# Kernel tuning notes

Hardware: AMD Instinct MI355X
Metric: run time of the kernel (lower is better)

The kernel has to match this reference:

```python
import jax, jax.numpy as jnp
import numpy as np

B, N, C, IN, H, G, OUT = 128, 256, 4, 64, 128, 8, 1
NUM_GNN_LAYERS = 2  # num_layers - 1


def setup_inputs() -> dict:
    key = jax.random.key(0)
    k1, k2, k3, k4, k5, k6 = jax.random.split(key, 6)
    V = jax.random.normal(k1, (B, N, IN), dtype=jnp.float32)
    A = jax.random.uniform(k2, (B, N, C, N), dtype=jnp.float32)
    mol_size = jax.random.randint(k3, (B,), 16, N + 1)  # at least 16 real nodes
    W_in = jax.random.normal(k4, (2, H, IN, G), dtype=jnp.float32) / np.float32(np.sqrt(IN) * np.sqrt(G))
    W_g = jax.random.normal(k5, (NUM_GNN_LAYERS, 2, H, H, G), dtype=jnp.float32) / np.float32(np.sqrt(H) * np.sqrt(G))
    W_out = jax.random.normal(k6, (2, OUT, H, 1), dtype=jnp.float32) / np.float32(np.sqrt(H))
    b_out = jnp.zeros((1, OUT), dtype=jnp.float32)
    return {"V": V, "A": A, "mol_size": mol_size, "W_in": W_in, "W_g": W_g, "W_out": W_out, "b_out": b_out}


def _kan_linear(x, W, bias=None):
    # x: [..., in], W: [2, out, in, grid]
    g = W.shape[-1]
    k = jnp.arange(1, g + 1, dtype=x.dtype)  # [g]
    xk = x[..., None] * k                    # [..., in, g]
    y = jnp.einsum('...ik,oik->...o', jnp.cos(xk), W[0]) \
      + jnp.einsum('...ik,oik->...o', jnp.sin(xk), W[1])
    if bias is not None:
        y = y + bias
    return y


def _kan_gnn_layer(h, A, W):
    # h: [b,n,in], A: [b,n,c,m], W: [2,out,in,grid]
    g = W.shape[-1]
    k = jnp.arange(1, g + 1, dtype=h.dtype)
    xk = h[..., None] * k                      # [b,n,in,g]
    f = jnp.einsum('bnik,oik->bno', jnp.cos(xk), W[0]) \
      + jnp.einsum('bnik,oik->bno', jnp.sin(xk), W[1])  # fourier_feat [b,n,out]
    # torch chain permute/reshape/bmm/sum(c) == sum_{n,c} A[b,n,c,m] * f[b,n,o]
    return jnp.einsum('bncm,bno->bmo', A, f)   # [b,m,out]


def reference(V, A, mol_size, W_in, W_g, W_out, b_out):
    h = _kan_linear(V, W_in)                   # [B,N,H]
    for i in range(W_g.shape[0]):
        m = _kan_gnn_layer(h, A, W_g[i])
        h = jax.nn.leaky_relu(m + h, negative_slope=0.01)
    # avg pooling over the first mol_size[i] (real) nodes per graph
    node_mask = (jnp.arange(N) < mol_size[:, None]).astype(h.dtype)  # [B,N]
    summed = jnp.einsum('bnh,bn->bh', h, node_mask)
    y = summed / mol_size[:, None].astype(h.dtype)                    # [B,H]
    out = jax.nn.sigmoid(_kan_linear(y, W_out, b_out))                # [B,OUT]
    return out
```

## Files before the change

kernel.cpp:

```cpp
#include <hip/hip_runtime.h>
#include <math.h>

namespace {
constexpr int B_ = 128;
constexpr int N_ = 256;
constexpr int H_ = 128;
constexpr int M_TOTAL = B_ * N_;
}

#define AS1 __attribute__((address_space(1)))
#define AS3 __attribute__((address_space(3)))

__device__ __forceinline__ void gl_lds16(const float* g, float* l) {
  __builtin_amdgcn_global_load_lds((const AS1 unsigned int*)g,
                                   (AS3 unsigned int*)l, 16, 0, 0);
}

template<int I, int O>
__global__ __launch_bounds__(256)
void wtr_kernel(const float* __restrict__ in, float* __restrict__ out) {
  int idx = blockIdx.x * 256 + threadIdx.x;
  constexpr int TOTAL = 2 * O * I * 8;
  if (idx >= TOTAL) return;
  int g = idx & 7;
  int t = idx >> 3;
  int i = t % I;
  int t2 = t / I;
  int o = t2 % O;
  int s = t2 / O;
  out[(size_t)((i * 8 + g) * 2 + s) * O + o] = in[idx];
}

template<int IN>
__global__ __launch_bounds__(256, 4)
void fourier3(const float* __restrict__ x,
              const float* __restrict__ Wt,
              float* __restrict__ out)
{
  constexpr int PAIRS = IN * 8;
  constexpr int CHUNKS = PAIRS / 16;
  __shared__ alignas(16) float wl[2][16][2][128];
  __shared__ alignas(16) float fC[2][16][64];
  __shared__ alignas(16) float fS[2][16][64];

  const int tid = threadIdx.x;
  const int node0 = blockIdx.x * 64;
  const int og = tid & 15;
  const int ng = tid >> 4;
  const int lane = tid & 63;
  const int wave = tid >> 6;
  const int il = tid >> 6;
  const int nd = tid & 63;

  float acc[4][8];
  #pragma unroll
  for (int a = 0; a < 4; ++a)
    #pragma unroll
    for (int b = 0; b < 8; ++b) acc[a][b] = 0.f;

  float xnext = 0.f;
  if (tid < 128) {
    float xv = x[(size_t)(node0 + nd) * IN + il];
    float s1, c1;
    sincosf(xv, &s1, &c1);
    float ckm = 1.f, skm = 0.f, ck = c1, sk = s1;
    #pragma unroll
    for (int g = 0; g < 8; ++g) {
      fC[0][il * 8 + g][nd] = ck;
      fS[0][il * 8 + g][nd] = sk;
      float cn = 2.f * c1 * ck - ckm, sn = 2.f * c1 * sk - skm;
      ckm = ck; skm = sk; ck = cn; sk = sn;
    }
    if (CHUNKS > 1) xnext = x[(size_t)(node0 + nd) * IN + 2 + il];
  } else {
    const int wv = wave - 2;
    #pragma unroll
    for (int q = 0; q < 8; ++q) {
      int u = (wv * 8 + q) * 64 + lane;
      gl_lds16(Wt + (size_t)u * 4,
               &wl[0][0][0][0] + (size_t)(wv * 8 + q) * 256);
    }
  }
  __syncthreads();

  int p = 0;
  for (int ic = 0; ic < CHUNKS; ++ic) {
    const int pn = p ^ 1;
    const bool more = (ic + 1 < CHUNKS);
    if (more) {
      if (tid < 128) {
        float s1, c1;
        sincosf(xnext, &s1, &c1);
        float ckm = 1.f, skm = 0.f, ck = c1, sk = s1;
        #pragma unroll
        for (int g = 0; g < 8; ++g) {
          fC[pn][il * 8 + g][nd] = ck;
          fS[pn][il * 8 + g][nd] = sk;
          float cn = 2.f * c1 * ck - ckm, sn = 2.f * c1 * sk - skm;
          ckm = ck; skm = sk; ck = cn; sk = sn;
        }
        if (ic + 2 < CHUNKS)
          xnext = x[(size_t)(node0 + nd) * IN + (ic + 2) * 2 + il];
      } else {
        const int wv = wave - 2;
        const float* wsrc = Wt + (size_t)(ic + 1) * 4096;
        float* wdst = &wl[pn][0][0][0];
        #pragma unroll
        for (int q = 0; q < 8; ++q) {
          int u = (wv * 8 + q) * 64 + lane;
          gl_lds16(wsrc + (size_t)u * 4, wdst + (size_t)(wv * 8 + q) * 256);
        }
      }
    }
    #pragma unroll 2
    for (int j = 0; j < 16; ++j) {
      float4 fc = *(const float4*)&fC[p][j][ng * 4];
      float4 fs = *(const float4*)&fS[p][j][ng * 4];
      float4 w0a = *(const float4*)&wl[p][j][0][og * 4];
      float4 w0b = *(const float4*)&wl[p][j][0][og * 4 + 64];
      float4 w1a = *(const float4*)&wl[p][j][1][og * 4];
      float4 w1b = *(const float4*)&wl[p][j][1][og * 4 + 64];
      float fcv[4] = {fc.x, fc.y, fc.z, fc.w};
      float fsv[4] = {fs.x, fs.y, fs.z, fs.w};
      float wa0[4] = {w0a.x, w0a.y, w0a.z, w0a.w};
      float wb0[4] = {w0b.x, w0b.y, w0b.z, w0b.w};
      float wa1[4] = {w1a.x, w1a.y, w1a.z, w1a.w};
      float wb1[4] = {w1b.x, w1b.y, w1b.z, w1b.w};
      #pragma unroll
      for (int nd2 = 0; nd2 < 4; ++nd2) {
        #pragma unroll
        for (int oo = 0; oo < 4; ++oo) {
          acc[nd2][oo]     += fcv[nd2] * wa0[oo] + fsv[nd2] * wa1[oo];
          acc[nd2][4 + oo] += fcv[nd2] * wb0[oo] + fsv[nd2] * wb1[oo];
        }
      }
    }
    __syncthreads();
    p ^= 1;
  }

  #pragma unroll
  for (int nd2 = 0; nd2 < 4; ++nd2) {
    int row = node0 + ng * 4 + nd2;
    float4 ra = {acc[nd2][0], acc[nd2][1], acc[nd2][2], acc[nd2][3]};
    float4 rb = {acc[nd2][4], acc[nd2][5], acc[nd2][6], acc[nd2][7]};
    *(float4*)&out[(size_t)row * H_ + og * 4] = ra;
    *(float4*)&out[(size_t)row * H_ + og * 4 + 64] = rb;
  }
}

__global__ __launch_bounds__(256)
void agg2(const float* __restrict__ A,
          const float* __restrict__ f,
          const float* __restrict__ h_in,
          float* __restrict__ h_out)
{
  __shared__ alignas(16) float As[2][32][64];
  __shared__ alignas(16) float fsh[2][8][128];
  const int tid = threadIdx.x;
  const int b = blockIdx.x >> 2;
  const int m0 = (blockIdx.x & 3) * 64;
  const int og = tid & 15;
  const int mg = tid >> 4;
  const int wave = tid >> 6;

  float acc[4][8];
  #pragma unroll
  for (int i = 0; i < 4; ++i)
    #pragma unroll
    for (int j = 0; j < 8; ++j) acc[i][j] = 0.f;

  const float* Ab = A + (size_t)b * (N_ * 4 * N_) + m0;
  const float* fb = f + (size_t)b * (N_ * H_);

  #pragma unroll
  for (int q = 0; q < 2; ++q) {
    int v = q * 256 + tid;
    gl_lds16(Ab + (size_t)(v >> 4) * N_ + (v & 15) * 4,
             &As[0][0][0] + (size_t)(q * 256 + wave * 64) * 4);
  }
  gl_lds16(fb + (size_t)(tid >> 5) * H_ + (tid & 31) * 4,
           &fsh[0][0][0] + (size_t)(wave * 64) * 4);
  __syncthreads();

  int p = 0;
  for (int ch = 0; ch < 32; ++ch) {
    const int pn = p ^ 1;
    if (ch + 1 < 32) {
      const float* Asrc = Ab + (size_t)(ch + 1) * 32 * N_;
      #pragma unroll
      for (int q = 0; q < 2; ++q) {
        int v = q * 256 + tid;
        gl_lds16(Asrc + (size_t)(v >> 4) * N_ + (v & 15) * 4,
                 &As[pn][0][0] + (size_t)(q * 256 + wave * 64) * 4);
      }
      gl_lds16(fb + (size_t)((ch + 1) * 8 + (tid >> 5)) * H_ + (tid & 31) * 4,
               &fsh[pn][0][0] + (size_t)(wave * 64) * 4);
    }
    #pragma unroll
    for (int kk = 0; kk < 32; ++kk) {
      float4 a  = *(const float4*)&As[p][kk][mg * 4];
      float4 f0 = *(const float4*)&fsh[p][kk >> 2][og * 4];
      float4 f1 = *(const float4*)&fsh[p][kk >> 2][og * 4 + 64];
      float av[4] = {a.x, a.y, a.z, a.w};
      float fo[8] = {f0.x, f0.y, f0.z, f0.w, f1.x, f1.y, f1.z, f1.w};
      #pragma unroll
      for (int mi = 0; mi < 4; ++mi)
        #pragma unroll
        for (int oi = 0; oi < 8; ++oi)
          acc[mi][oi] += av[mi] * fo[oi];
    }
    __syncthreads();
    p ^= 1;
  }

  #pragma unroll
  for (int mi = 0; mi < 4; ++mi) {
    int row = b * N_ + m0 + mg * 4 + mi;
    const float* hr = &h_in[(size_t)row * H_];
    float* ho = &h_out[(size_t)row * H_];
    float4 r0 = *(const float4*)&hr[og * 4];
    float4 r1 = *(const float4*)&hr[og * 4 + 64];
    float4 o0, o1;
    float v;
    v = acc[mi][0] + r0.x; o0.x = v >= 0.f ? v : 0.01f * v;
    v = acc[mi][1] + r0.y; o0.y = v >= 0.f ? v : 0.01f * v;
    v = acc[mi][2] + r0.z; o0.z = v >= 0.f ? v : 0.01f * v;
    v = acc[mi][3] + r0.w; o0.w = v >= 0.f ? v : 0.01f * v;
    v = acc[mi][4] + r1.x; o1.x = v >= 0.f ? v : 0.01f * v;
    v = acc[mi][5] + r1.y; o1.y = v >= 0.f ? v : 0.01f * v;
    v = acc[mi][6] + r1.z; o1.z = v >= 0.f ? v : 0.01f * v;
    v = acc[mi][7] + r1.w; o1.w = v >= 0.f ? v : 0.01f * v;
    *(float4*)&ho[og * 4] = o0;
    *(float4*)&ho[og * 4 + 64] = o1;
  }
}

__global__ __launch_bounds__(128)
void pool_kernel(const float* __restrict__ h,
                 const int* __restrict__ mol,
                 const float* __restrict__ Wout,
                 const float* __restrict__ bout,
                 float* __restrict__ out)
{
  __shared__ float red[128];
  const int b = blockIdx.x;
  const int t = threadIdx.x;
  const int ms = mol[b];
  const float* hb = h + (size_t)b * N_ * H_;
  float sum = 0.f;
  for (int n = 0; n < ms; ++n) sum += hb[(size_t)n * H_ + t];
  float y = sum / (float)ms;
  float s1, c1;
  sincosf(y, &s1, &c1);
  red[t] = c1 * Wout[t] + s1 * Wout[H_ + t];
  __syncthreads();
  for (int sft = 64; sft > 0; sft >>= 1) {
    if (t < sft) red[t] += red[t + sft];
    __syncthreads();
  }
  if (t == 0) {
    float z = red[0] + bout[0];
    out[b] = 1.f / (1.f + expf(-z));
  }
}

extern "C" void kernel_launch(void* const* d_in, const int* in_sizes, int n_in,
                              void* d_out, int out_size, void* d_ws, size_t ws_size,
                              hipStream_t stream) {
  const float* V    = (const float*)d_in[0];
  const float* A    = (const float*)d_in[1];
  const int*   mol  = (const int*)d_in[2];
  const float* Win  = (const float*)d_in[3];
  const float* Wg   = (const float*)d_in[4];
  const float* Wout = (const float*)d_in[5];
  const float* bout = (const float*)d_in[6];
  float* out = (float*)d_out;

  float* h     = (float*)d_ws;
  float* f     = h  + (size_t)M_TOTAL * H_;
  float* h2    = f  + (size_t)M_TOTAL * H_;
  float* wt_in = h2 + (size_t)M_TOTAL * H_;
  float* wt_g0 = wt_in + 512 * 2 * H_;
  float* wt_g1 = wt_g0 + 1024 * 2 * H_;

  wtr_kernel<64, 128><<<(2 * 128 * 64 * 8) / 256, 256, 0, stream>>>(Win, wt_in);
  wtr_kernel<128, 128><<<(2 * 128 * 128 * 8) / 256, 256, 0, stream>>>(Wg, wt_g0);
  wtr_kernel<128, 128><<<(2 * 128 * 128 * 8) / 256, 256, 0, stream>>>(
      Wg + (size_t)2 * 128 * 128 * 8, wt_g1);

  fourier3<64><<<M_TOTAL / 64, 256, 0, stream>>>(V, wt_in, h);

  float* hc = h;
  float* hn = h2;
  const float* wt_g[2] = {wt_g0, wt_g1};
  for (int l = 0; l < 2; ++l) {
    fourier3<128><<<M_TOTAL / 64, 256, 0, stream>>>(hc, wt_g[l], f);
    agg2<<<B_ * 4, 256, 0, stream>>>(A, f, hc, hn);
    float* tmp = hc; hc = hn; hn = tmp;
  }

  pool_kernel<<<B_, 128, 0, stream>>>(hc, mol, Wout, bout, out);
}
```

Measured before the change: 967.4 us.

## Split Fourier feature reduction across two blocks and sum partials in aggregation

Measured after the change: 1.006 ms. 1.04x slower.

```diff
diff --git a/kernel.cpp b/kernel.cpp
--- a/kernel.cpp
+++ b/kernel.cpp
@@ -31,26 +31,44 @@
   out[(size_t)((i * 8 + g) * 2 + s) * O + o] = in[idx];
 }
 
+__global__ __launch_bounds__(256)
+void add4_kernel(const float* __restrict__ a, const float* __restrict__ b,
+                 float* __restrict__ o, int n4) {
+  int i = blockIdx.x * 256 + threadIdx.x;
+  int stride = gridDim.x * 256;
+  for (; i < n4; i += stride) {
+    float4 x = ((const float4*)a)[i];
+    float4 y = ((const float4*)b)[i];
+    float4 r = {x.x + y.x, x.y + y.y, x.z + y.z, x.w + y.w};
+    ((float4*)o)[i] = r;
+  }
+}
+
 template<int IN>
 __global__ __launch_bounds__(256, 4)
-void fourier3(const float* __restrict__ x,
+void fourier4(const float* __restrict__ x,
               const float* __restrict__ Wt,
-              float* __restrict__ out)
+              float* __restrict__ out0,
+              float* __restrict__ out1)
 {
-  constexpr int PAIRS = IN * 8;
-  constexpr int CHUNKS = PAIRS / 16;
-  __shared__ alignas(16) float wl[2][16][2][128];
-  __shared__ alignas(16) float fC[2][16][64];
-  __shared__ alignas(16) float fS[2][16][64];
+  constexpr int HP = IN * 4;
+  constexpr int CHUNKS = HP / 8;
+  __shared__ alignas(16) float wl[2][8][2][128];
+  __shared__ alignas(16) float fC[2][8][64];
+  __shared__ alignas(16) float fS[2][8][64];
 
   const int tid = threadIdx.x;
-  const int node0 = blockIdx.x * 64;
+  const int khalf = blockIdx.x & 1;
+  const int node0 = (blockIdx.x >> 1) * 64;
   const int og = tid & 15;
   const int ng = tid >> 4;
   const int lane = tid & 63;
   const int wave = tid >> 6;
-  const int il = tid >> 6;
   const int nd = tid & 63;
+
+  float* __restrict__ out = khalf ? out1 : out0;
+  const float* wb = Wt + (size_t)khalf * HP * 256;
+  const float* xrow = x + (size_t)(node0 + nd) * IN + khalf * (IN / 2);
 
   float acc[4][8];
   #pragma unroll
@@ -58,27 +76,22 @@
     #pragma unroll
     for (int b = 0; b < 8; ++b) acc[a][b] = 0.f;
 
-  float xnext = 0.f;
-  if (tid < 128) {
-    float xv = x[(size_t)(node0 + nd) * IN + il];
+  float xv = xrow[0];
+  float xnext = (CHUNKS > 1) ? xrow[1] : 0.f;
+  #pragma unroll
+  for (int q = 0; q < 2; ++q) {
+    int bw = wave * 2 + q;
+    gl_lds16(wb + (size_t)(bw * 64 + lane) * 4, &wl[0][0][0][0] + bw * 256);
+  }
+  {
     float s1, c1;
     sincosf(xv, &s1, &c1);
     float ckm = 1.f, skm = 0.f, ck = c1, sk = s1;
     #pragma unroll
     for (int g = 0; g < 8; ++g) {
-      fC[0][il * 8 + g][nd] = ck;
-      fS[0][il * 8 + g][nd] = sk;
+      if ((g >> 1) == wave) { fC[0][g][nd] = ck; fS[0][g][nd] = sk; }
       float cn = 2.f * c1 * ck - ckm, sn = 2.f * c1 * sk - skm;
       ckm = ck; skm = sk; ck = cn; sk = sn;
-    }
-    if (CHUNKS > 1) xnext = x[(size_t)(node0 + nd) * IN + 2 + il];
-  } else {
-    const int wv = wave - 2;
-    #pragma unroll
-    for (int q = 0; q < 8; ++q) {
-      int u = (wv * 8 + q) * 64 + lane;
-      gl_lds16(Wt + (size_t)u * 4,
-               &wl[0][0][0][0] + (size_t)(wv * 8 + q) * 256);
     }
   }
   __syncthreads();
@@ -88,32 +101,26 @@
     const int pn = p ^ 1;
     const bool more = (ic + 1 < CHUNKS);
     if (more) {
-      if (tid < 128) {
-        float s1, c1;
-        sincosf(xnext, &s1, &c1);
-        float ckm = 1.f, skm = 0.f, ck = c1, sk = s1;
-        #pragma unroll
-        for (int g = 0; g < 8; ++g) {
-          fC[pn][il * 8 + g][nd] = ck;
-          fS[pn][il * 8 + g][nd] = sk;
-          float cn = 2.f * c1 * ck - ckm, sn = 2.f * c1 * sk - skm;
-          ckm = ck; skm = sk; ck = cn; sk = sn;
-        }
-        if (ic + 2 < CHUNKS)
-          xnext = x[(size_t)(node0 + nd) * IN + (ic + 2) * 2 + il];
-      } else {
-        const int wv = wave - 2;
-        const float* wsrc = Wt + (size_t)(ic + 1) * 4096;
-        float* wdst = &wl[pn][0][0][0];
-        #pragma unroll
-        for (int q = 0; q < 8; ++q) {
-          int u = (wv * 8 + q) * 64 + lane;
-          gl_lds16(wsrc + (size_t)u * 4, wdst + (size_t)(wv * 8 + q) * 256);
-        }
+      const float* wsrc = wb + (size_t)(ic + 1) * 2048;
+      #pragma unroll
+      for (int q = 0; q < 2; ++q) {
+        int bw = wave * 2 + q;
+        gl_lds16(wsrc + (size_t)(bw * 64 + lane) * 4,
+                 &wl[pn][0][0][0] + bw * 256);
       }
-    }
-    #pragma unroll 2
-    for (int j = 0; j < 16; ++j) {
+      float s1, c1;
+      sincosf(xnext, &s1, &c1);
+      float ckm = 1.f, skm = 0.f, ck = c1, sk = s1;
+      #pragma unroll
+      for (int g = 0; g < 8; ++g) {
+        if ((g >> 1) == wave) { fC[pn][g][nd] = ck; fS[pn][g][nd] = sk; }
+        float cn = 2.f * c1 * ck - ckm, sn = 2.f * c1 * sk - skm;
+        ckm = ck; skm = sk; ck = cn; sk = sn;
+      }
+      if (ic + 2 < CHUNKS) xnext = xrow[ic + 2];
+    }
+    #pragma unroll 4
+    for (int j = 0; j < 8; ++j) {
       float4 fc = *(const float4*)&fC[p][j][ng * 4];
       float4 fs = *(const float4*)&fS[p][j][ng * 4];
       float4 w0a = *(const float4*)&wl[p][j][0][og * 4];
@@ -150,8 +157,9 @@
 }
 
 __global__ __launch_bounds__(256)
-void agg2(const float* __restrict__ A,
-          const float* __restrict__ f,
+void agg3(const float* __restrict__ A,
+          const float* __restrict__ f0,
+          const float* __restrict__ f1,
           const float* __restrict__ h_in,
           float* __restrict__ h_out)
 {
@@ -163,6 +171,8 @@
   const int og = tid & 15;
   const int mg = tid >> 4;
   const int wave = tid >> 6;
+  const int fr = tid >> 5;
+  const int fc4 = (tid & 31) * 4;
 
   float acc[4][8];
   #pragma unroll
@@ -170,23 +180,31 @@
     #pragma unroll
     for (int j = 0; j < 8; ++j) acc[i][j] = 0.f;
 
-  const float* Ab = A + (size_t)b * (N_ * 4 * N_) + m0;
-  const float* fb = f + (size_t)b * (N_ * H_);
-
+  const float* Ab  = A  + (size_t)b * (N_ * 4 * N_) + m0;
+  const float* f0b = f0 + (size_t)b * (N_ * H_);
+  const float* f1b = f1 + (size_t)b * (N_ * H_);
+
+  float4 u0 = *(const float4*)(f0b + (size_t)fr * H_ + fc4);
+  float4 u1 = *(const float4*)(f1b + (size_t)fr * H_ + fc4);
   #pragma unroll
   for (int q = 0; q < 2; ++q) {
     int v = q * 256 + tid;
     gl_lds16(Ab + (size_t)(v >> 4) * N_ + (v & 15) * 4,
              &As[0][0][0] + (size_t)(q * 256 + wave * 64) * 4);
   }
-  gl_lds16(fb + (size_t)(tid >> 5) * H_ + (tid & 31) * 4,
-           &fsh[0][0][0] + (size_t)(wave * 64) * 4);
+  {
+    float4 s = {u0.x + u1.x, u0.y + u1.y, u0.z + u1.z, u0.w + u1.w};
+    *(float4*)&fsh[0][fr][fc4] = s;
+  }
   __syncthreads();
 
   int p = 0;
   for (int ch = 0; ch < 32; ++ch) {
     const int pn = p ^ 1;
+    float4 v0, v1;
     if (ch + 1 < 32) {
+      v0 = *(const float4*)(f0b + (size_t)((ch + 1) * 8 + fr) * H_ + fc4);
+      v1 = *(const float4*)(f1b + (size_t)((ch + 1) * 8 + fr) * H_ + fc4);
       const float* Asrc = Ab + (size_t)(ch + 1) * 32 * N_;
       #pragma unroll
       for (int q = 0; q < 2; ++q) {
@@ -194,21 +212,23 @@
         gl_lds16(Asrc + (size_t)(v >> 4) * N_ + (v & 15) * 4,
                  &As[pn][0][0] + (size_t)(q * 256 + wave * 64) * 4);
       }
-      gl_lds16(fb + (size_t)((ch + 1) * 8 + (tid >> 5)) * H_ + (tid & 31) * 4,
-               &fsh[pn][0][0] + (size_t)(wave * 64) * 4);
     }
     #pragma unroll
     for (int kk = 0; kk < 32; ++kk) {
       float4 a  = *(const float4*)&As[p][kk][mg * 4];
-      float4 f0 = *(const float4*)&fsh[p][kk >> 2][og * 4];
-      float4 f1 = *(const float4*)&fsh[p][kk >> 2][og * 4 + 64];
+      float4 g0 = *(const float4*)&fsh[p][kk >> 2][og * 4];
+      float4 g1 = *(const float4*)&fsh[p][kk >> 2][og * 4 + 64];
       float av[4] = {a.x, a.y, a.z, a.w};
-      float fo[8] = {f0.x, f0.y, f0.z, f0.w, f1.x, f1.y, f1.z, f1.w};
+      float fo[8] = {g0.x, g0.y, g0.z, g0.w, g1.x, g1.y, g1.z, g1.w};
       #pragma unroll
       for (int mi = 0; mi < 4; ++mi)
         #pragma unroll
         for (int oi = 0; oi < 8; ++oi)
           acc[mi][oi] += av[mi] * fo[oi];
+    }
+    if (ch + 1 < 32) {
+      float4 s = {v0.x + v1.x, v0.y + v1.y, v0.z + v1.z, v0.w + v1.w};
+      *(float4*)&fsh[pn][fr][fc4] = s;
     }
     __syncthreads();
     p ^= 1;
@@ -277,10 +297,12 @@
   const float* bout = (const float*)d_in[6];
   float* out = (float*)d_out;
 
+  const size_t BUF = (size_t)M_TOTAL * H_;
   float* h     = (float*)d_ws;
-  float* f     = h  + (size_t)M_TOTAL * H_;
-  float* h2    = f  + (size_t)M_TOTAL * H_;
-  float* wt_in = h2 + (size_t)M_TOTAL * H_;
+  float* h2    = h  + BUF;
+  float* f0    = h2 + BUF;
+  float* f1    = f0 + BUF;
+  float* wt_in = f1 + BUF;
   float* wt_g0 = wt_in + 512 * 2 * H_;
   float* wt_g1 = wt_g0 + 1024 * 2 * H_;
 
@@ -289,14 +311,15 @@
   wtr_kernel<128, 128><<<(2 * 128 * 128 * 8) / 256, 256, 0, stream>>>(
       Wg + (size_t)2 * 128 * 128 * 8, wt_g1);
 
-  fourier3<64><<<M_TOTAL / 64, 256, 0, stream>>>(V, wt_in, h);
+  fourier4<64><<<(M_TOTAL / 64) * 2, 256, 0, stream>>>(V, wt_in, f0, f1);
+  add4_kernel<<<2048, 256, 0, stream>>>(f0, f1, h, (int)(BUF / 4));
 
   float* hc = h;
   float* hn = h2;
   const float* wt_g[2] = {wt_g0, wt_g1};
   for (int l = 0; l < 2; ++l) {
-    fourier3<128><<<M_TOTAL / 64, 256, 0, stream>>>(hc, wt_g[l], f);
-    agg2<<<B_ * 4, 256, 0, stream>>>(A, f, hc, hn);
+    fourier4<128><<<(M_TOTAL / 64) * 2, 256, 0, stream>>>(hc, wt_g[l], f0, f1);
+    agg3<<<B_ * 4, 256, 0, stream>>>(A, f0, f1, hc, hn);
     float* tmp = hc; hc = hn; hn = tmp;
   }
 
```
